# Optimization experiments

Hardware: AMD Instinct MI355X
Metric: run time of the kernel (lower is better)

## Reference

```python
import jax, jax.numpy as jnp
import numpy as np
from jax import lax

TRAJ_STEPS = 50  # output_dim=100 -> 50 (x,y) waypoints


def setup_inputs() -> dict:
    key = jax.random.key(0)
    ks = jax.random.split(key, 12)
    s = 0.05  # small init scale to keep gates out of saturation
    return {
        "x": jax.random.normal(ks[0], (32768, 256), jnp.float32),
        "W1": jax.random.normal(ks[1], (256, 64), jnp.float32) * s,
        "b1": jax.random.normal(ks[2], (64,), jnp.float32) * s,
        "W2": jax.random.normal(ks[3], (64, 64), jnp.float32) * s,
        "b2": jax.random.normal(ks[4], (64,), jnp.float32) * s,
        "Wih": jax.random.normal(ks[5], (2, 192), jnp.float32) * s,   # GRU input weights, gate order (r,z,n)
        "bih": jax.random.normal(ks[6], (192,), jnp.float32) * s,
        "Whh": jax.random.normal(ks[7], (64, 192), jnp.float32) * s,  # GRU hidden weights
        "bhh": jax.random.normal(ks[8], (192,), jnp.float32) * s,
        "Wout": jax.random.normal(ks[9], (64, 2), jnp.float32) * s,
        "bout": jax.random.normal(ks[10], (2,), jnp.float32) * s,
    }


def _forward(x, W1, b1, W2, b2, Wih, bih, Whh, bhh, Wout, bout):
    H = W2.shape[1]
    # backbone MLP -> initial hidden state
    z = jax.nn.relu(x @ W1 + b1)
    z = jax.nn.relu(z @ W2 + b2)  # [B, H]

    def step(carry, _):
        wp, h = carry                      # wp: [B,2] current waypoint, h: [B,H]
        gi = wp @ Wih + bih                # [B, 3H]
        gh = h @ Whh + bhh                 # [B, 3H]
        ir, iz, inn = gi[..., :H], gi[..., H:2 * H], gi[..., 2 * H:]
        hr, hz, hn = gh[..., :H], gh[..., H:2 * H], gh[..., 2 * H:]
        r = jax.nn.sigmoid(ir + hr)
        u = jax.nn.sigmoid(iz + hz)
        n = jnp.tanh(inn + r * hn)
        h_new = (1.0 - u) * n + u * h      # PyTorch GRUCell update
        dx = jax.nn.sigmoid(h_new @ Wout + bout)  # [B,2]
        wp_new = wp + dx                   # residual accumulation
        return (wp_new, h_new), wp_new

    wp0 = jnp.zeros(x.shape[:-1] + (2,), z.dtype)
    _, wps = lax.scan(step, (wp0, z), None, length=TRAJ_STEPS)  # [T, B, 2]
    wps = jnp.moveaxis(wps, 0, -2)                              # [B, T, 2]
    return wps.reshape(x.shape[:-1] + (2 * TRAJ_STEPS,))        # [B, 2T]


def reference(x, W1, b1, W2, b2, Wih, bih, Whh, bhh, Wout, bout):
    return _forward(x, W1, b1, W2, b2, Wih, bih, Whh, bhh, Wout, bout)
```

## Files before the change

kernel.cpp:

```cpp
#include <hip/hip_runtime.h>
#include <hip/hip_bf16.h>

#define TRAJ 50

typedef __attribute__((ext_vector_type(8))) short short8;
typedef __attribute__((ext_vector_type(4))) float f32x4;
typedef __attribute__((ext_vector_type(2))) float f32x2;

#if defined(__has_builtin)
#if __has_builtin(__builtin_amdgcn_exp2f)
#define EXP2F(x) __builtin_amdgcn_exp2f(x)
#else
#define EXP2F(x) exp2f(x)
#endif
#if __has_builtin(__builtin_amdgcn_rcpf)
#define RCPF(x) __builtin_amdgcn_rcpf(x)
#else
#define RCPF(x) (1.0f/(x))
#endif
#else
#define EXP2F(x) exp2f(x)
#define RCPF(x) (1.0f/(x))
#endif

#define BAR() asm volatile("s_waitcnt lgkmcnt(0)\n\ts_barrier" ::: "memory")

__device__ __forceinline__ unsigned short f2bf(float f){
  union { float f; unsigned u; } v; v.f = f;
  unsigned u = v.u;
  u += 0x7FFFu + ((u >> 16) & 1u);
  return (unsigned short)(u >> 16);
}
__device__ __forceinline__ unsigned pk(unsigned short a, unsigned short b){
  return (unsigned)a | ((unsigned)b << 16);
}
__device__ __forceinline__ unsigned pkbf(float a, float b){
  union { __hip_bfloat162 h; unsigned u; } c;
  c.h = __float22bfloat162_rn(make_float2(a, b));
  return c.u;
}
__device__ __forceinline__ short8 mkfrag(uint2 v){
  union { unsigned u[4]; short8 s; } c;
  c.u[0] = v.x; c.u[1] = v.y; c.u[2] = 0u; c.u[3] = 0u;
  return c.s;
}

#define MFMA16(A,B,C) __builtin_amdgcn_mfma_f32_16x16x32_bf16((A),(B),(C),0,0,0)

#define SSC (-1.44269504f)
#define TSC ( 2.88539008f)

__device__ __forceinline__ f32x2 exp2v(f32x2 v){ return (f32x2){EXP2F(v[0]), EXP2F(v[1])}; }
__device__ __forceinline__ f32x2 rcpv (f32x2 v){ return (f32x2){RCPF(v[0]), RCPF(v[1])}; }

__device__ __forceinline__ f32x2 gru_pair(f32x2 r_, f32x2 u_, f32x2 n_, f32x2 i_, f32x2 hp){
  const f32x2 one = (f32x2){1.f, 1.f};
  f32x2 d1 = exp2v(r_) + one;
  f32x2 d2 = exp2v(u_) + one;
  f32x2 rp = rcpv(d1 * d2);
  f32x2 rv = d2 * rp;
  f32x2 uv = d1 * rp;
  f32x2 y  = __builtin_elementwise_fma(rv, n_, i_);
  f32x2 nv = one - 2.f * rcpv(exp2v(y) + one);
  return __builtin_elementwise_fma(uv, hp - nv, nv);
}

__device__ __forceinline__ short8 gatherA(const float* __restrict__ M, int N,
                                          int k0, int i, float scale){
  const float* q = M + (size_t)k0 * N + i;
  union { unsigned u[4]; short8 s; } c;
  #pragma unroll
  for (int j = 0; j < 4; ++j){
    float a = q[(2*j  ) * N];
    float b = q[(2*j+1) * N];
    c.u[j] = pk(f2bf(scale * a), f2bf(scale * b));
  }
  return c.s;
}

__global__ __launch_bounds__(128, 3) void gru_actor_kernel(
    const float* __restrict__ x,
    const float* __restrict__ W1, const float* __restrict__ b1,
    const float* __restrict__ W2, const float* __restrict__ b2,
    const float* __restrict__ Wih, const float* __restrict__ bih,
    const float* __restrict__ Whh, const float* __restrict__ bhh,
    const float* __restrict__ Wout, const float* __restrict__ bout,
    float* __restrict__ out)
{
  __shared__ __align__(16) char sm_h[4096];

  const int t    = threadIdx.x;
  const int p    = t >> 6;
  const int l    = t & 63;
  const int lr   = l & 15;
  const int lg   = l >> 4;
  const int rowbase = blockIdx.x * 16;
  const int swz  = (lr & 7) << 4;

  f32x4 accL[2];
  #pragma unroll
  for (int tql = 0; tql < 2; ++tql){
    float4 bv = *(const float4*)(b1 + 16 * (2*p + tql) + 4 * lg);
    accL[tql] = (f32x4){bv.x, bv.y, bv.z, bv.w};
  }
  {
    const float* xrow = x + (size_t)(rowbase + lr) * 256;
    #pragma unroll
    for (int kb = 0; kb < 8; ++kb){
      int k0 = kb * 32 + lg * 8;
      float4 xa = *(const float4*)(xrow + k0);
      float4 xb = *(const float4*)(xrow + k0 + 4);
      union { unsigned u[4]; short8 s; } bc;
      bc.u[0] = pkbf(xa.x, xa.y); bc.u[1] = pkbf(xa.z, xa.w);
      bc.u[2] = pkbf(xb.x, xb.y); bc.u[3] = pkbf(xb.z, xb.w);
      #pragma unroll
      for (int tql = 0; tql < 2; ++tql){
        short8 A = gatherA(W1, 64, k0, 16 * (2*p + tql) + lr, 1.0f);
        accL[tql] = MFMA16(A, bc.s, accL[tql]);
      }
    }
  }
  #pragma unroll
  for (int tql = 0; tql < 2; ++tql){
    f32x4 a0 = accL[tql];
    *(uint2*)(sm_h + lr * 128 + ((64 * p + 32 * tql + 8 * lg) ^ swz)) =
        make_uint2(pkbf(fmaxf(a0[0],0.f), fmaxf(a0[1],0.f)), pkbf(fmaxf(a0[2],0.f), fmaxf(a0[3],0.f)));
  }
  __syncthreads();

  f32x2 h2[4];
  {
    f32x4 acc2[2];
    #pragma unroll
    for (int tql = 0; tql < 2; ++tql){
      float4 bv = *(const float4*)(b2 + 16 * (2*p + tql) + 4 * lg);
      acc2[tql] = (f32x4){bv.x, bv.y, bv.z, bv.w};
    }
    #pragma unroll
    for (int kb = 0; kb < 2; ++kb){
      short8 B = *(const short8*)(sm_h + lr * 128 + ((kb * 64 + lg * 16) ^ swz));
      #pragma unroll
      for (int tql = 0; tql < 2; ++tql){
        short8 A = gatherA(W2, 64, kb * 32 + lg * 8, 16 * (2*p + tql) + lr, 1.0f);
        acc2[tql] = MFMA16(A, B, acc2[tql]);
      }
    }
    h2[0] = (f32x2){fmaxf(acc2[0][0],0.f), fmaxf(acc2[0][1],0.f)};
    h2[1] = (f32x2){fmaxf(acc2[0][2],0.f), fmaxf(acc2[0][3],0.f)};
    h2[2] = (f32x2){fmaxf(acc2[1][0],0.f), fmaxf(acc2[1][1],0.f)};
    h2[3] = (f32x2){fmaxf(acc2[1][2],0.f), fmaxf(acc2[1][3],0.f)};
    __syncthreads();
    *(uint2*)(sm_h + 2048 + lr * 128 + ((64 * p + 0  + 8 * lg) ^ swz)) =
        make_uint2(pkbf(h2[0][0], h2[0][1]), pkbf(h2[1][0], h2[1][1]));
    *(uint2*)(sm_h + 2048 + lr * 128 + ((64 * p + 32 + 8 * lg) ^ swz)) =
        make_uint2(pkbf(h2[2][0], h2[2][1]), pkbf(h2[3][0], h2[3][1]));
  }

  short8 Ah[3][2][2];
  #pragma unroll
  for (int g = 0; g < 3; ++g){
    float s = (g < 2) ? SSC : TSC;
    #pragma unroll
    for (int tql = 0; tql < 2; ++tql){
      int i = g * 64 + 32 * p + 16 * tql + lr;
      #pragma unroll
      for (int kb = 0; kb < 2; ++kb)
        Ah[g][tql][kb] = gatherA(Whh, 192, kb * 32 + lg * 8, i, s);
    }
  }
  uint2 Ak2p[4][2] = {};
  if (lg == 0){
    #pragma unroll
    for (int tql = 0; tql < 2; ++tql){
      int dr = 32 * p + 16 * tql + lr;
      int du = 64 + dr, dn = 128 + dr;
      Ak2p[0][tql] = make_uint2(pk(f2bf(SSC*Wih[dr]), f2bf(SSC*Wih[192+dr])),
                                pk(f2bf(SSC*(bih[dr]+bhh[dr])), 0));
      Ak2p[1][tql] = make_uint2(pk(f2bf(SSC*Wih[du]), f2bf(SSC*Wih[192+du])),
                                pk(f2bf(SSC*(bih[du]+bhh[du])), 0));
      Ak2p[2][tql] = make_uint2(0u, pk(f2bf(TSC*bhh[dn]), 0));
      Ak2p[3][tql] = make_uint2(pk(f2bf(TSC*Wih[dn]), f2bf(TSC*Wih[192+dn])),
                                pk(f2bf(TSC*bih[dn]), 0));
    }
  }
  short8 AoR[2];
  #pragma unroll
  for (int kb = 0; kb < 2; ++kb){
    short8 f = (short8){0,0,0,0,0,0,0,0};
    if (lr < 2){
      #pragma unroll
      for (int j = 0; j < 8; ++j){
        int k = kb * 32 + lg * 8 + j;
        f[j] = (short)f2bf(SSC * Wout[k * 2 + lr]);
      }
    }
    AoR[kb] = f;
  }
  const float bo0 = SSC * bout[0], bo1 = SSC * bout[1];
  __syncthreads();

  float wp0 = 0.f, wp1 = 0.f;
  float* outp = out + (size_t)(rowbase + lr) * 100;
  short8 B0 = *(const short8*)(sm_h + 2048 + lr * 128 + ((0  + lg * 16) ^ swz));
  short8 B1 = *(const short8*)(sm_h + 2048 + lr * 128 + ((64 + lg * 16) ^ swz));

  #pragma unroll 2
  for (int s = 0; s < TRAJ; ++s){
    char* bufW = sm_h + ((s & 1) << 11);
    short8 B2;
    {
      unsigned b2lo = 0u, b2hi = 0u;
      if (lg == 0){ b2lo = pkbf(wp0, wp1); b2hi = 0x00003F80u; }
      union { unsigned u[4]; short8 sv; } c;
      c.u[0] = b2lo; c.u[1] = b2hi; c.u[2] = 0u; c.u[3] = 0u;
      B2 = c.sv;
    }
    #pragma unroll
    for (int tql = 0; tql < 2; ++tql){
      f32x4 aR = (f32x4){0,0,0,0}, aU = (f32x4){0,0,0,0};
      f32x4 aN = (f32x4){0,0,0,0}, aI = (f32x4){0,0,0,0};
      aR = MFMA16(Ah[0][tql][0], B0, aR);
      aR = MFMA16(Ah[0][tql][1], B1, aR);
      aR = MFMA16(mkfrag(Ak2p[0][tql]), B2, aR);
      aU = MFMA16(Ah[1][tql][0], B0, aU);
      aU = MFMA16(Ah[1][tql][1], B1, aU);
      aU = MFMA16(mkfrag(Ak2p[1][tql]), B2, aU);
      aN = MFMA16(Ah[2][tql][0], B0, aN);
      aN = MFMA16(Ah[2][tql][1], B1, aN);
      aN = MFMA16(mkfrag(Ak2p[2][tql]), B2, aN);
      aI = MFMA16(mkfrag(Ak2p[3][tql]), B2, aI);
      f32x2 hA = gru_pair((f32x2){aR[0],aR[1]}, (f32x2){aU[0],aU[1]},
                          (f32x2){aN[0],aN[1]}, (f32x2){aI[0],aI[1]}, h2[2*tql+0]);
      f32x2 hB = gru_pair((f32x2){aR[2],aR[3]}, (f32x2){aU[2],aU[3]},
                          (f32x2){aN[2],aN[3]}, (f32x2){aI[2],aI[3]}, h2[2*tql+1]);
      h2[2*tql+0] = hA; h2[2*tql+1] = hB;
      *(uint2*)(bufW + lr * 128 + ((64 * p + 32 * tql + 8 * lg) ^ swz)) =
          make_uint2(pkbf(hA[0], hA[1]), pkbf(hB[0], hB[1]));
    }
    BAR();
    short8 nB0 = *(const short8*)(bufW + lr * 128 + ((0  + lg * 16) ^ swz));
    short8 nB1 = *(const short8*)(bufW + lr * 128 + ((64 + lg * 16) ^ swz));
    f32x4 aD = (f32x4){0,0,0,0};
    if (lg == 0){ aD[0] = bo0; aD[1] = bo1; }
    aD = MFMA16(AoR[0], nB0, aD);
    aD = MFMA16(AoR[1], nB1, aD);
    if (lg == 0){
      float ea = EXP2F(aD[0]), eb = EXP2F(aD[1]);
      float da = 1.f + ea, db = 1.f + eb;
      float rp = RCPF(da * db);
      wp0 += db * rp;
      wp1 += da * rp;
      if (p == 0) *(float2*)(outp + 2 * s) = make_float2(wp0, wp1);
    }
    B0 = nB0; B1 = nB1;
  }
}

extern "C" void kernel_launch(void* const* d_in, const int* in_sizes, int n_in,
                              void* d_out, int out_size, void* d_ws, size_t ws_size,
                              hipStream_t stream) {
  (void)n_in; (void)out_size; (void)d_ws; (void)ws_size;
  const float* x    = (const float*)d_in[0];
  const float* W1   = (const float*)d_in[1];
  const float* b1   = (const float*)d_in[2];
  const float* W2   = (const float*)d_in[3];
  const float* b2   = (const float*)d_in[4];
  const float* Wih  = (const float*)d_in[5];
  const float* bih  = (const float*)d_in[6];
  const float* Whh  = (const float*)d_in[7];
  const float* bhh  = (const float*)d_in[8];
  const float* Wout = (const float*)d_in[9];
  const float* bout = (const float*)d_in[10];
  float* out = (float*)d_out;

  int nrows = in_sizes[0] / 256;
  int grid  = nrows / 16;
  gru_actor_kernel<<<dim3(grid), dim3(128), 0, stream>>>(
      x, W1, b1, W2, b2, Wih, bih, Whh, bhh, Wout, bout, out);
}
```

Measured before the change: 131.7 us.

## Split GRU hidden dims across four waves, two row groups per block

Each block now has 512 threads processing two 16-row groups. Within a group, four waves each own 16 hidden dimensions instead of two waves each owning 32. This halves per-wave MFMA work and register footprint per recurrent step, raising parallelism on the serial 50-step chain. The cost is more waves synchronising at each step's barrier, block-wide barriers coupling the two row groups, and redundant wp computation in all lanes.

Result: faster. 115.4 us (-12.3%).

```diff
diff --git a/kernel.cpp b/kernel.cpp
--- a/kernel.cpp
+++ b/kernel.cpp
@@ -67,18 +67,18 @@
 
 __device__ __forceinline__ short8 gatherA(const float* __restrict__ M, int N,
                                           int k0, int i, float scale){
-  const float* q = M + (size_t)k0 * N + i;
+  const float* qp = M + (size_t)k0 * N + i;
   union { unsigned u[4]; short8 s; } c;
   #pragma unroll
   for (int j = 0; j < 4; ++j){
-    float a = q[(2*j  ) * N];
-    float b = q[(2*j+1) * N];
+    float a = qp[(2*j  ) * N];
+    float b = qp[(2*j+1) * N];
     c.u[j] = pk(f2bf(scale * a), f2bf(scale * b));
   }
   return c.s;
 }
 
-__global__ __launch_bounds__(128, 3) void gru_actor_kernel(
+__global__ __launch_bounds__(512, 4) void gru_actor_kernel(
     const float* __restrict__ x,
     const float* __restrict__ W1, const float* __restrict__ b1,
     const float* __restrict__ W2, const float* __restrict__ b2,
@@ -87,22 +87,23 @@
     const float* __restrict__ Wout, const float* __restrict__ bout,
     float* __restrict__ out)
 {
-  __shared__ __align__(16) char sm_h[4096];
+  __shared__ __align__(16) char sm_h[8192];
 
   const int t    = threadIdx.x;
-  const int p    = t >> 6;
+  const int q    = (t >> 6) & 3;
+  const int grp  = t >> 8;
   const int l    = t & 63;
   const int lr   = l & 15;
   const int lg   = l >> 4;
-  const int rowbase = blockIdx.x * 16;
+  const int rowbase = blockIdx.x * 32 + grp * 16;
+  const int dimq = q * 16;
   const int swz  = (lr & 7) << 4;
-
-  f32x4 accL[2];
-  #pragma unroll
-  for (int tql = 0; tql < 2; ++tql){
-    float4 bv = *(const float4*)(b1 + 16 * (2*p + tql) + 4 * lg);
-    accL[tql] = (f32x4){bv.x, bv.y, bv.z, bv.w};
-  }
+  char* base = sm_h + (grp << 12);
+  const int colw = 32 * q + 8 * lg;
+
+  f32x4 acc1;
+  { float4 bv = *(const float4*)(b1 + dimq + 4 * lg);
+    acc1 = (f32x4){bv.x, bv.y, bv.z, bv.w}; }
   {
     const float* xrow = x + (size_t)(rowbase + lr) * 256;
     #pragma unroll
@@ -113,75 +114,50 @@
       union { unsigned u[4]; short8 s; } bc;
       bc.u[0] = pkbf(xa.x, xa.y); bc.u[1] = pkbf(xa.z, xa.w);
       bc.u[2] = pkbf(xb.x, xb.y); bc.u[3] = pkbf(xb.z, xb.w);
-      #pragma unroll
-      for (int tql = 0; tql < 2; ++tql){
-        short8 A = gatherA(W1, 64, k0, 16 * (2*p + tql) + lr, 1.0f);
-        accL[tql] = MFMA16(A, bc.s, accL[tql]);
-      }
-    }
-  }
-  #pragma unroll
-  for (int tql = 0; tql < 2; ++tql){
-    f32x4 a0 = accL[tql];
-    *(uint2*)(sm_h + lr * 128 + ((64 * p + 32 * tql + 8 * lg) ^ swz)) =
-        make_uint2(pkbf(fmaxf(a0[0],0.f), fmaxf(a0[1],0.f)), pkbf(fmaxf(a0[2],0.f), fmaxf(a0[3],0.f)));
-  }
+      short8 A = gatherA(W1, 64, k0, dimq + lr, 1.0f);
+      acc1 = MFMA16(A, bc.s, acc1);
+    }
+  }
+  *(uint2*)(base + lr * 128 + (colw ^ swz)) =
+      make_uint2(pkbf(fmaxf(acc1[0],0.f), fmaxf(acc1[1],0.f)),
+                 pkbf(fmaxf(acc1[2],0.f), fmaxf(acc1[3],0.f)));
   __syncthreads();
 
-  f32x2 h2[4];
+  f32x2 h2[2];
   {
-    f32x4 acc2[2];
-    #pragma unroll
-    for (int tql = 0; tql < 2; ++tql){
-      float4 bv = *(const float4*)(b2 + 16 * (2*p + tql) + 4 * lg);
-      acc2[tql] = (f32x4){bv.x, bv.y, bv.z, bv.w};
-    }
+    f32x4 acc2;
+    float4 bv = *(const float4*)(b2 + dimq + 4 * lg);
+    acc2 = (f32x4){bv.x, bv.y, bv.z, bv.w};
     #pragma unroll
     for (int kb = 0; kb < 2; ++kb){
-      short8 B = *(const short8*)(sm_h + lr * 128 + ((kb * 64 + lg * 16) ^ swz));
-      #pragma unroll
-      for (int tql = 0; tql < 2; ++tql){
-        short8 A = gatherA(W2, 64, kb * 32 + lg * 8, 16 * (2*p + tql) + lr, 1.0f);
-        acc2[tql] = MFMA16(A, B, acc2[tql]);
-      }
-    }
-    h2[0] = (f32x2){fmaxf(acc2[0][0],0.f), fmaxf(acc2[0][1],0.f)};
-    h2[1] = (f32x2){fmaxf(acc2[0][2],0.f), fmaxf(acc2[0][3],0.f)};
-    h2[2] = (f32x2){fmaxf(acc2[1][0],0.f), fmaxf(acc2[1][1],0.f)};
-    h2[3] = (f32x2){fmaxf(acc2[1][2],0.f), fmaxf(acc2[1][3],0.f)};
-    __syncthreads();
-    *(uint2*)(sm_h + 2048 + lr * 128 + ((64 * p + 0  + 8 * lg) ^ swz)) =
+      short8 B = *(const short8*)(base + lr * 128 + ((kb * 64 + 16 * lg) ^ swz));
+      short8 A = gatherA(W2, 64, kb * 32 + lg * 8, dimq + lr, 1.0f);
+      acc2 = MFMA16(A, B, acc2);
+    }
+    h2[0] = (f32x2){fmaxf(acc2[0],0.f), fmaxf(acc2[1],0.f)};
+    h2[1] = (f32x2){fmaxf(acc2[2],0.f), fmaxf(acc2[3],0.f)};
+    *(uint2*)(base + 2048 + lr * 128 + (colw ^ swz)) =
         make_uint2(pkbf(h2[0][0], h2[0][1]), pkbf(h2[1][0], h2[1][1]));
-    *(uint2*)(sm_h + 2048 + lr * 128 + ((64 * p + 32 + 8 * lg) ^ swz)) =
-        make_uint2(pkbf(h2[2][0], h2[2][1]), pkbf(h2[3][0], h2[3][1]));
-  }
-
-  short8 Ah[3][2][2];
+  }
+
+  short8 Ah[3][2];
   #pragma unroll
   for (int g = 0; g < 3; ++g){
-    float s = (g < 2) ? SSC : TSC;
+    float sc = (g < 2) ? SSC : TSC;
     #pragma unroll
-    for (int tql = 0; tql < 2; ++tql){
-      int i = g * 64 + 32 * p + 16 * tql + lr;
-      #pragma unroll
-      for (int kb = 0; kb < 2; ++kb)
-        Ah[g][tql][kb] = gatherA(Whh, 192, kb * 32 + lg * 8, i, s);
-    }
-  }
-  uint2 Ak2p[4][2] = {};
+    for (int kb = 0; kb < 2; ++kb)
+      Ah[g][kb] = gatherA(Whh, 192, kb * 32 + lg * 8, g * 64 + dimq + lr, sc);
+  }
+  uint2 Ak2p[4] = {};
   if (lg == 0){
-    #pragma unroll
-    for (int tql = 0; tql < 2; ++tql){
-      int dr = 32 * p + 16 * tql + lr;
-      int du = 64 + dr, dn = 128 + dr;
-      Ak2p[0][tql] = make_uint2(pk(f2bf(SSC*Wih[dr]), f2bf(SSC*Wih[192+dr])),
-                                pk(f2bf(SSC*(bih[dr]+bhh[dr])), 0));
-      Ak2p[1][tql] = make_uint2(pk(f2bf(SSC*Wih[du]), f2bf(SSC*Wih[192+du])),
-                                pk(f2bf(SSC*(bih[du]+bhh[du])), 0));
-      Ak2p[2][tql] = make_uint2(0u, pk(f2bf(TSC*bhh[dn]), 0));
-      Ak2p[3][tql] = make_uint2(pk(f2bf(TSC*Wih[dn]), f2bf(TSC*Wih[192+dn])),
-                                pk(f2bf(TSC*bih[dn]), 0));
-    }
+    int dr = dimq + lr, du = 64 + dr, dn = 128 + dr;
+    Ak2p[0] = make_uint2(pk(f2bf(SSC*Wih[dr]), f2bf(SSC*Wih[192+dr])),
+                         pk(f2bf(SSC*(bih[dr]+bhh[dr])), 0));
+    Ak2p[1] = make_uint2(pk(f2bf(SSC*Wih[du]), f2bf(SSC*Wih[192+du])),
+                         pk(f2bf(SSC*(bih[du]+bhh[du])), 0));
+    Ak2p[2] = make_uint2(0u, pk(f2bf(TSC*bhh[dn]), 0));
+    Ak2p[3] = make_uint2(pk(f2bf(TSC*Wih[dn]), f2bf(TSC*Wih[192+dn])),
+                         pk(f2bf(TSC*bih[dn]), 0));
   }
   short8 AoR[2];
   #pragma unroll
@@ -201,12 +177,12 @@
 
   float wp0 = 0.f, wp1 = 0.f;
   float* outp = out + (size_t)(rowbase + lr) * 100;
-  short8 B0 = *(const short8*)(sm_h + 2048 + lr * 128 + ((0  + lg * 16) ^ swz));
-  short8 B1 = *(const short8*)(sm_h + 2048 + lr * 128 + ((64 + lg * 16) ^ swz));
+  short8 B0 = *(const short8*)(base + 2048 + lr * 128 + ((0  + 16 * lg) ^ swz));
+  short8 B1 = *(const short8*)(base + 2048 + lr * 128 + ((64 + 16 * lg) ^ swz));
 
   #pragma unroll 2
   for (int s = 0; s < TRAJ; ++s){
-    char* bufW = sm_h + ((s & 1) << 11);
+    char* bufW = base + ((s & 1) << 11);
     short8 B2;
     {
       unsigned b2lo = 0u, b2hi = 0u;
@@ -215,43 +191,41 @@
       c.u[0] = b2lo; c.u[1] = b2hi; c.u[2] = 0u; c.u[3] = 0u;
       B2 = c.sv;
     }
-    #pragma unroll
-    for (int tql = 0; tql < 2; ++tql){
-      f32x4 aR = (f32x4){0,0,0,0}, aU = (f32x4){0,0,0,0};
-      f32x4 aN = (f32x4){0,0,0,0}, aI = (f32x4){0,0,0,0};
-      aR = MFMA16(Ah[0][tql][0], B0, aR);
-      aR = MFMA16(Ah[0][tql][1], B1, aR);
-      aR = MFMA16(mkfrag(Ak2p[0][tql]), B2, aR);
-      aU = MFMA16(Ah[1][tql][0], B0, aU);
-      aU = MFMA16(Ah[1][tql][1], B1, aU);
-      aU = MFMA16(mkfrag(Ak2p[1][tql]), B2, aU);
-      aN = MFMA16(Ah[2][tql][0], B0, aN);
-      aN = MFMA16(Ah[2][tql][1], B1, aN);
-      aN = MFMA16(mkfrag(Ak2p[2][tql]), B2, aN);
-      aI = MFMA16(mkfrag(Ak2p[3][tql]), B2, aI);
-      f32x2 hA = gru_pair((f32x2){aR[0],aR[1]}, (f32x2){aU[0],aU[1]},
-                          (f32x2){aN[0],aN[1]}, (f32x2){aI[0],aI[1]}, h2[2*tql+0]);
-      f32x2 hB = gru_pair((f32x2){aR[2],aR[3]}, (f32x2){aU[2],aU[3]},
-                          (f32x2){aN[2],aN[3]}, (f32x2){aI[2],aI[3]}, h2[2*tql+1]);
-      h2[2*tql+0] = hA; h2[2*tql+1] = hB;
-      *(uint2*)(bufW + lr * 128 + ((64 * p + 32 * tql + 8 * lg) ^ swz)) =
-          make_uint2(pkbf(hA[0], hA[1]), pkbf(hB[0], hB[1]));
-    }
+    f32x4 aR = (f32x4){0,0,0,0}, aU = (f32x4){0,0,0,0};
+    f32x4 aN = (f32x4){0,0,0,0}, aI = (f32x4){0,0,0,0};
+    aR = MFMA16(Ah[0][0], B0, aR);
+    aR = MFMA16(Ah[0][1], B1, aR);
+    aR = MFMA16(mkfrag(Ak2p[0]), B2, aR);
+    aU = MFMA16(Ah[1][0], B0, aU);
+    aU = MFMA16(Ah[1][1], B1, aU);
+    aU = MFMA16(mkfrag(Ak2p[1]), B2, aU);
+    aN = MFMA16(Ah[2][0], B0, aN);
+    aN = MFMA16(Ah[2][1], B1, aN);
+    aN = MFMA16(mkfrag(Ak2p[2]), B2, aN);
+    aI = MFMA16(mkfrag(Ak2p[3]), B2, aI);
+    f32x2 hA = gru_pair((f32x2){aR[0],aR[1]}, (f32x2){aU[0],aU[1]},
+                        (f32x2){aN[0],aN[1]}, (f32x2){aI[0],aI[1]}, h2[0]);
+    f32x2 hB = gru_pair((f32x2){aR[2],aR[3]}, (f32x2){aU[2],aU[3]},
+                        (f32x2){aN[2],aN[3]}, (f32x2){aI[2],aI[3]}, h2[1]);
+    h2[0] = hA; h2[1] = hB;
+    *(uint2*)(bufW + lr * 128 + (colw ^ swz)) =
+        make_uint2(pkbf(hA[0], hA[1]), pkbf(hB[0], hB[1]));
     BAR();
-    short8 nB0 = *(const short8*)(bufW + lr * 128 + ((0  + lg * 16) ^ swz));
-    short8 nB1 = *(const short8*)(bufW + lr * 128 + ((64 + lg * 16) ^ swz));
+    short8 nB0 = *(const short8*)(bufW + lr * 128 + ((0  + 16 * lg) ^ swz));
+    short8 nB1 = *(const short8*)(bufW + lr * 128 + ((64 + 16 * lg) ^ swz));
     f32x4 aD = (f32x4){0,0,0,0};
     if (lg == 0){ aD[0] = bo0; aD[1] = bo1; }
     aD = MFMA16(AoR[0], nB0, aD);
     aD = MFMA16(AoR[1], nB1, aD);
-    if (lg == 0){
+    {
       float ea = EXP2F(aD[0]), eb = EXP2F(aD[1]);
       float da = 1.f + ea, db = 1.f + eb;
       float rp = RCPF(da * db);
       wp0 += db * rp;
       wp1 += da * rp;
-      if (p == 0) *(float2*)(outp + 2 * s) = make_float2(wp0, wp1);
-    }
+    }
+    if (lg == 0 && q == 0)
+      *(float2*)(outp + 2 * s) = make_float2(wp0, wp1);
     B0 = nB0; B1 = nB1;
   }
 }
@@ -274,7 +248,7 @@
   float* out = (float*)d_out;
 
   int nrows = in_sizes[0] / 256;
-  int grid  = nrows / 16;
-  gru_actor_kernel<<<dim3(grid), dim3(128), 0, stream>>>(
+  int grid  = nrows / 32;
+  gru_actor_kernel<<<dim3(grid), dim3(512), 0, stream>>>(
       x, W1, b1, W2, b2, Wih, bih, Whh, bhh, Wout, bout, out);
 }
```
